# Performance work log

Measured on AMD Instinct MI355X. Metric: run time of the kernel, lower is better.

The kernel has to match this reference:

```python
import jax, jax.numpy as jnp
from jax import lax
import numpy as np

B, ENC, H, DE, T = 16384, 512, 256, 32, 64


def setup_inputs() -> dict:
    key = jax.random.key(0)
    ks = jax.random.split(key, 12)
    s = lambda fan: 1.0 / np.sqrt(fan)
    return {
        "encoded_input_series": jax.random.normal(ks[0], (B, ENC), jnp.float32),
        "final_x_val": jax.random.normal(ks[1], (B, 1), jnp.float32),
        # embed_func: Dense(DE) applied to scalar input (last dim = 1)
        "W_emb": jax.random.normal(ks[2], (1, DE), jnp.float32) * s(1),
        "b_emb": jnp.zeros((DE,), jnp.float32),
        # encode_reshape layer: Dense(H) on encoded series -> initial h
        "W_enc": jax.random.normal(ks[3], (ENC, H), jnp.float32) * s(ENC),
        "b_enc": jnp.zeros((H,), jnp.float32),
        # LSTM cell params (Keras gate order i, f, c, o)
        "W_k": jax.random.normal(ks[4], (DE, 4 * H), jnp.float32) * s(DE),
        "W_r": jax.random.normal(ks[5], (H, 4 * H), jnp.float32) * s(H),
        "b_lstm": jnp.concatenate([jnp.zeros((H,)), jnp.ones((H,)), jnp.zeros((2 * H,))]).astype(jnp.float32),
        # reduce layer: Dense(1)
        "W_red": jax.random.normal(ks[6], (H, 1), jnp.float32) * s(H),
        "b_red": jnp.zeros((1,), jnp.float32),
        "decode_length": T,
    }


def reference(encoded_input_series, final_x_val, W_emb, b_emb, W_enc, b_enc,
              W_k, W_r, b_lstm, W_red, b_red, decode_length):
    Hdim = W_r.shape[0]
    # initial hidden state from encoder summary; cell state zero-initialized
    h0 = encoded_input_series @ W_enc + b_enc            # [B, H]
    c0 = jnp.zeros_like(h0)
    # initial decoder input: embed of last observed value
    x0 = final_x_val @ W_emb + b_emb                     # [B, DE]

    def step(carry, _):
        h, c, x = carry
        gates = x @ W_k + h @ W_r + b_lstm               # [B, 4H]
        i, f, cb, o = jnp.split(gates, 4, axis=-1)
        c_new = jax.nn.sigmoid(f) * c + jax.nn.sigmoid(i) * jnp.tanh(cb)
        h_new = jax.nn.sigmoid(o) * jnp.tanh(c_new)
        y = h_new @ W_red + b_red                        # [B, 1]
        x_next = y @ W_emb + b_emb
        return (h_new, c_new, x_next), y[:, 0]

    _, ys = lax.scan(step, (h0, c0, x0), None, length=decode_length)
    return ys.T                                          # [B, T]
```

## Files before the change

### kernel.cpp

```cpp
#include <hip/hip_runtime.h>
#include <hip/hip_bf16.h>
#include <math.h>


typedef _Float16 f16x8 __attribute__((ext_vector_type(8)));
typedef float f32x4 __attribute__((ext_vector_type(4)));

#define DEV __device__ __forceinline__

constexpr int ENC = 512;
constexpr int HD  = 256;
constexpr int DE  = 32;
constexpr int TT  = 64;
constexpr int NG  = 4 * HD;
constexpr int NKT = 8;
constexpr int TS  = 528;
constexpr int BR  = 32;
constexpr int NMT = 2;
constexpr int BPS = 12;
constexpr int WRS = 36;

constexpr float L2E = 1.44269504088896f;

DEV bool is_f32(const void* blstm) {
  return ((const unsigned*)blstm)[256] == 0x3F800000u;
}
DEV float ldf(const void* p, size_t i, bool f32) {
  return f32 ? ((const float*)p)[i]
             : __bfloat162float(((const __hip_bfloat16*)p)[i]);
}
DEV float gscale(int n) {
  return ((n >> 8) == 2) ? (2.0f * L2E) : L2E;
}
DEV void split2h(float v, _Float16& hi, _Float16& lo) {
  hi = (_Float16)v;
  lo = (_Float16)(v - (float)hi);
}
DEV void ld8cvt2h(const void* p, size_t i, bool f32, f16x8& hi, f16x8& lo) {
  if (f32) {
    const f32x4* q = (const f32x4*)((const float*)p + i);
    f32x4 u0 = q[0], u1 = q[1];
#pragma unroll
    for (int j = 0; j < 4; ++j) {
      float a = u0[j], b = u1[j];
      _Float16 ah = (_Float16)a, bh = (_Float16)b;
      hi[j] = ah; hi[4 + j] = bh;
      lo[j] = (_Float16)(a - (float)ah); lo[4 + j] = (_Float16)(b - (float)bh);
    }
  } else {
    const __hip_bfloat16* s = (const __hip_bfloat16*)p + i;
#pragma unroll
    for (int j = 0; j < 8; ++j) {
      float a = __bfloat162float(s[j]);
      _Float16 ah = (_Float16)a;
      hi[j] = ah;
      lo[j] = (_Float16)(a - (float)ah);
    }
  }
}
DEV f16x8 load8h(const _Float16* p) {
  return *reinterpret_cast<const f16x8*>(p);
}

DEV void waitflag(volatile int* f, int v) {
  while (*f < v) { __builtin_amdgcn_s_sleep(1); }
  asm volatile("" ::: "memory");
}
DEV void signalflag(volatile int* f, int v, int lane) {
  asm volatile("s_waitcnt lgkmcnt(0)" ::: "memory");
  if (lane == 0) *f = v;
}

__global__ __launch_bounds__(256) void pack_vec(const void* __restrict__ wemb,
                                                const void* __restrict__ bemb,
                                                const void* __restrict__ wk,
                                                const void* __restrict__ bl,
                                                const void* __restrict__ bredp,
                                                float* __restrict__ wk2n,
                                                float* __restrict__ wk2s,
                                                float* __restrict__ bps,
                                                float* __restrict__ bp2P) {
  const bool f32 = is_f32(bl);
  int n = blockIdx.x * 256 + threadIdx.x;
  if (n >= NG) return;
  float s1 = 0.f, s2 = 0.f;
  for (int j = 0; j < DE; ++j) {
    float wkv = ldf(wk, (size_t)j * NG + n, f32);
    s1 += ldf(wemb, j, f32) * wkv;
    s2 += ldf(bemb, j, f32) * wkv;
  }
  float b = s2 + ldf(bl, n, f32);
  float sc = gscale(n);
  wk2n[n] = s1;
  wk2s[n] = s1 * sc;
  bps[n]  = b * sc;
  int g = n >> 8, rem = n & 255;
  int hh = (rem >> 4) & 1;
  int cbase = (rem & 0xE0) | (rem & 15);
  int nf = g * 2 + hh;
  bp2P[cbase * BPS + nf] = (b + ldf(bredp, 0, f32) * s1) * sc;
}

__global__ __launch_bounds__(256) void pack_w(const void* __restrict__ wr,
                                              const void* __restrict__ bl,
                                              const void* __restrict__ wred,
                                              const float* __restrict__ wk2n,
                                              _Float16* __restrict__ d0,
                                              _Float16* __restrict__ d1) {
  const bool f32 = is_f32(bl);
  int idx = blockIdx.x * 256 + threadIdx.x;
  if (idx >= NKT * 64 * 64) return;
  int lane = idx & 63, tile = idx >> 6;
  int nt = tile & 63, ks = tile >> 6;
  int kb = ks * 32 + ((lane >> 4) << 3);
  int n  = (nt << 4) + (lane & 15);
  float wn = wk2n[n];
  float sc = gscale(n);
#pragma unroll
  for (int j = 0; j < 8; ++j) {
    int k = kb + j;
    float v = ldf(wr, (size_t)k * NG + n, f32);
    d0[idx * 8 + j] = (_Float16)(v * sc);
    d1[idx * 8 + j] = (_Float16)((v + ldf(wred, k, f32) * wn) * sc);
  }
}

__global__ __launch_bounds__(256) void pack_e(const void* __restrict__ we,
                                              const void* __restrict__ bl,
                                              _Float16* __restrict__ dhi,
                                              _Float16* __restrict__ dlo) {
  const bool f32 = is_f32(bl);
  int idx = blockIdx.x * 256 + threadIdx.x;
  if (idx >= 16 * 16 * 64) return;
  int lane = idx & 63, tile = idx >> 6;
  int nt = tile & 15, ks = tile >> 4;
  int kb = ks * 32 + ((lane >> 4) << 3);
  int n  = (nt << 4) + (lane & 15);
#pragma unroll
  for (int j = 0; j < 8; ++j) {
    float v = ldf(we, (size_t)(kb + j) * HD + n, f32);
    _Float16 h, l;
    split2h(v, h, l);
    dhi[idx * 8 + j] = h;
    dlo[idx * 8 + j] = l;
  }
}

__global__ __launch_bounds__(512)
__attribute__((amdgpu_waves_per_eu(4, 4)))
void lstm_main(
    const void* __restrict__ enc,
    const void* __restrict__ fx,
    const void* __restrict__ benc,
    const void* __restrict__ blstm,
    const void* __restrict__ wred,
    const void* __restrict__ bredp,
    const _Float16* __restrict__ pW0,
    const _Float16* __restrict__ pW1,
    const _Float16* __restrict__ pEhi,
    const _Float16* __restrict__ pElo,
    const float* __restrict__ wk2s,
    const float* __restrict__ bps,
    const float* __restrict__ bp2P,
    const int* __restrict__ dlen,
    void* __restrict__ out) {
  __shared__ __align__(16) _Float16 frag[2][NMT * NKT * TS];
  __shared__ __align__(16) float bp0L[NG];
  __shared__ __align__(16) float wk2L[NG];
  __shared__ __align__(16) float bp2P_l[HD * BPS];
  __shared__ __align__(16) float wredfP[16 * WRS];
  __shared__ __align__(16) float fxL[BR];
  __shared__ int flagv[NKT];

  const bool f32 = is_f32(blstm);
  const int tid  = threadIdx.x;
  const int w    = tid >> 6;
  const int lane = tid & 63;
  const int q    = lane >> 4;
  const int cl   = lane & 15;
  const int r0   = blockIdx.x * BR;
  int Tn = dlen[0];
  if (Tn < 1 || Tn > TT) Tn = TT;

  const int aoff = lane * 8;
  const int hwb = w * TS + q * 32 + 128 * (cl >> 3) + (cl & 7);
  const int cbase = w * 32 + cl;

  const int yrow  = tid >> 4, ypart = tid & 15;
  const int ybase = ((yrow >> 4) * NKT + (ypart >> 1)) * TS +
                    ((yrow & 15) + 16 * ((ypart & 1) * 2)) * 8;
  const int yws   = ypart * WRS;

  if (tid < HD) wredfP[(tid >> 4) * WRS + (tid & 15)] = ldf(wred, tid, f32);
  if (tid < BR) fxL[tid] = ldf(fx, r0 + tid, f32);
  if (tid < NKT) flagv[tid] = 0;
  bp0L[tid]        = bps[tid];
  bp0L[tid + 512]  = bps[tid + 512];
  wk2L[tid]        = wk2s[tid];
  wk2L[tid + 512]  = wk2s[tid + 512];
#pragma unroll
  for (int k = 0; k < HD * BPS / 512; ++k)
    bp2P_l[tid + k * 512] = bp2P[tid + k * 512];
  const float bredf = ldf(bredp, 0, f32);

  f32x4 acc0[NMT][2];
  {
    float be0 = ldf(benc, w * 32 + cl, f32);
    float be1 = ldf(benc, w * 32 + 16 + cl, f32);
#pragma unroll
    for (int mt = 0; mt < NMT; ++mt) {
      acc0[mt][0] = (f32x4){be0, be0, be0, be0};
      acc0[mt][1] = (f32x4){be1, be1, be1, be1};
    }
  }
  const size_t ebase = ((size_t)(w * 2) * 64 + lane) * 8;
#pragma unroll 1
  for (int ks = 0; ks < ENC / 32; ++ks) {
    f16x8 bh[2], bl2[2];
#pragma unroll
    for (int hh = 0; hh < 2; ++hh) {
      size_t fo = ebase + (size_t)(ks * 16 + hh) * 512;
      bh[hh]  = load8h(pEhi + fo);
      bl2[hh] = load8h(pElo + fo);
    }
#pragma unroll
    for (int mt = 0; mt < NMT; ++mt) {
      f16x8 ah, al;
      ld8cvt2h(enc, (size_t)(r0 + mt * 16 + cl) * ENC + ks * 32 + q * 8, f32, ah, al);
#pragma unroll
      for (int hh = 0; hh < 2; ++hh) {
        acc0[mt][hh] = __builtin_amdgcn_mfma_f32_16x16x32_f16(ah, bh[hh],  acc0[mt][hh], 0, 0, 0);
        acc0[mt][hh] = __builtin_amdgcn_mfma_f32_16x16x32_f16(al, bh[hh],  acc0[mt][hh], 0, 0, 0);
        acc0[mt][hh] = __builtin_amdgcn_mfma_f32_16x16x32_f16(ah, bl2[hh], acc0[mt][hh], 0, 0, 0);
      }
    }
  }
#pragma unroll
  for (int mt = 0; mt < NMT; ++mt)
#pragma unroll
    for (int hh = 0; hh < 2; ++hh)
#pragma unroll
      for (int r = 0; r < 4; ++r) {
        int idx = mt * NKT * TS + hwb + r * 8 + hh * 256;
        frag[0][idx] = (_Float16)acc0[mt][hh][r];
      }

  f32x4 cst[NMT][2];
#pragma unroll
  for (int mt = 0; mt < NMT; ++mt)
#pragma unroll
    for (int hh = 0; hh < 2; ++hh) cst[mt][hh] = (f32x4){0.f, 0.f, 0.f, 0.f};

  __syncthreads();

  const _Float16* wbase0 = pW0 + ((size_t)(w * 2) * 64 + lane) * 8;
  const _Float16* wbase1 = pW1 + ((size_t)(w * 2) * 64 + lane) * 8;

#pragma unroll 1
  for (int t = 0; t < Tn; ++t) {
    const _Float16* FH = &frag[t & 1][0];
    _Float16* WH = &frag[(t + 1) & 1][0];

    f32x4 acc[NMT][8];
    if (t == 0) {
      f32x4 fxv[NMT];
#pragma unroll
      for (int mt = 0; mt < NMT; ++mt)
        fxv[mt] = *(const f32x4*)&fxL[mt * 16 + q * 4];
#pragma unroll
      for (int nf = 0; nf < 8; ++nf) {
        int col = (nf >> 1) * 256 + (nf & 1) * 16 + cbase;
        float bb = bp0L[col], wv = wk2L[col];
#pragma unroll
        for (int mt = 0; mt < NMT; ++mt) {
          f32x4 a;
#pragma unroll
          for (int r = 0; r < 4; ++r) a[r] = bb + fxv[mt][r] * wv;
          acc[mt][nf] = a;
        }
      }
    } else {
      f32x4 bA = *(const f32x4*)&bp2P_l[cbase * BPS];
      f32x4 bB = *(const f32x4*)&bp2P_l[cbase * BPS + 4];
#pragma unroll
      for (int nf = 0; nf < 8; ++nf) {
        float bb = (nf < 4) ? bA[nf & 3] : bB[nf & 3];
#pragma unroll
        for (int mt = 0; mt < NMT; ++mt) acc[mt][nf] = (f32x4){bb, bb, bb, bb};
      }
    }

    const _Float16* wb = (t == 0) ? wbase0 : wbase1;
#pragma unroll 1
    for (int j = 0; j < 8; ++j) {
      int ks = (j + w) & 7;
      if (j > 0) waitflag(&flagv[ks], t);
#pragma unroll
      for (int half = 0; half < 2; ++half) {
        f16x8 bc[4];
#pragma unroll
        for (int p = 0; p < 4; ++p)
          bc[p] = load8h(wb +
                         (size_t)(ks * 64 + (half * 2 + (p >> 1)) * 16 + (p & 1)) * 512);
#pragma unroll
        for (int mt = 0; mt < NMT; ++mt) {
          f16x8 ah = load8h(&FH[(mt * NKT + ks) * TS + aoff]);
          __builtin_amdgcn_s_setprio(1);
#pragma unroll
          for (int p = 0; p < 4; ++p)
            acc[mt][half * 4 + p] =
                __builtin_amdgcn_mfma_f32_16x16x32_f16(ah, bc[p], acc[mt][half * 4 + p], 0, 0, 0);
          __builtin_amdgcn_s_setprio(0);
        }
      }
    }

    if (t > 0) {
      float sum = 0.f;
#pragma unroll
      for (int jj = 0; jj < 2; ++jj) {
        f16x8 hv = load8h(&FH[ybase + jj * 128]);
        f32x4 wv0 = *(const f32x4*)&wredfP[yws + jj * 8];
        f32x4 wv1 = *(const f32x4*)&wredfP[yws + jj * 8 + 4];
#pragma unroll
        for (int j = 0; j < 4; ++j) {
          sum += (float)hv[j] * wv0[j];
          sum += (float)hv[4 + j] * wv1[j];
        }
      }
      sum += __shfl_xor(sum, 1);
      sum += __shfl_xor(sum, 2);
      sum += __shfl_xor(sum, 4);
      sum += __shfl_xor(sum, 8);
      if (ypart == 0) {
        float y = sum + bredf;
        size_t oi = (size_t)(r0 + yrow) * TT + (t - 1);
        if (f32) ((float*)out)[oi] = y;
        else     ((__hip_bfloat16*)out)[oi] = __float2bfloat16(y);
      }
    }

#pragma unroll
    for (int mt = 0; mt < NMT; ++mt)
#pragma unroll
      for (int hh = 0; hh < 2; ++hh)
#pragma unroll
        for (int r = 0; r < 4; ++r) {
          float gi = acc[mt][0 + hh][r];
          float gf = acc[mt][2 + hh][r];
          float gc = acc[mt][4 + hh][r];
          float go = acc[mt][6 + hh][r];
          float P = __builtin_amdgcn_exp2f(-gi);
          float F = __builtin_amdgcn_exp2f(-gf);
          float Q = __builtin_amdgcn_exp2f(-gc);
          float S = __builtin_amdgcn_exp2f(-go);
          float p1 = 1.0f + P, q1 = 1.0f + Q, f1 = 1.0f + F, s1 = 1.0f + S;
          float pq = p1 * q1;
          float num = cst[mt][hh][r] * pq + (1.0f - Q) * f1;
          float cn  = num * __builtin_amdgcn_rcpf(f1 * pq);
          cst[mt][hh][r] = cn;
          float R = __builtin_amdgcn_exp2f(-2.0f * L2E * cn);
          float hn = (1.0f - R) * __builtin_amdgcn_rcpf(s1 * (1.0f + R));
          int idx = mt * NKT * TS + hwb + r * 8 + hh * 256;
          WH[idx] = (_Float16)hn;
        }
    signalflag(&flagv[w], t + 1, lane);
  }

#pragma unroll 1
  for (int s = 0; s < NKT; ++s) waitflag(&flagv[s], Tn);
  {
    const _Float16* FH = &frag[Tn & 1][0];
    float sum = 0.f;
#pragma unroll
    for (int jj = 0; jj < 2; ++jj) {
      f16x8 hv = load8h(&FH[ybase + jj * 128]);
      f32x4 wv0 = *(const f32x4*)&wredfP[yws + jj * 8];
      f32x4 wv1 = *(const f32x4*)&wredfP[yws + jj * 8 + 4];
#pragma unroll
      for (int j = 0; j < 4; ++j) {
        sum += (float)hv[j] * wv0[j];
        sum += (float)hv[4 + j] * wv1[j];
      }
    }
    sum += __shfl_xor(sum, 1);
    sum += __shfl_xor(sum, 2);
    sum += __shfl_xor(sum, 4);
    sum += __shfl_xor(sum, 8);
    if (ypart == 0) {
      float y = sum + bredf;
      size_t oi = (size_t)(r0 + yrow) * TT + (Tn - 1);
      if (f32) ((float*)out)[oi] = y;
      else     ((__hip_bfloat16*)out)[oi] = __float2bfloat16(y);
    }
  }
}

extern "C" void kernel_launch(void* const* d_in, const int* in_sizes, int n_in,
                              void* d_out, int out_size, void* d_ws, size_t ws_size,
                              hipStream_t stream) {
  const void* enc  = d_in[0];
  const void* fx   = d_in[1];
  const void* wemb = d_in[2];
  const void* bemb = d_in[3];
  const void* wenc = d_in[4];
  const void* benc = d_in[5];
  const void* wk   = d_in[6];
  const void* wr   = d_in[7];
  const void* bl   = d_in[8];
  const void* wred = d_in[9];
  const void* bred = d_in[10];
  const int* dlen  = (const int*)d_in[11];

  _Float16* pW0 = (_Float16*)d_ws;
  _Float16* pW1 = pW0 + NKT * 64 * 64 * 8;
  _Float16* pEhi = pW1 + NKT * 64 * 64 * 8;
  _Float16* pElo = pEhi + 16 * 16 * 64 * 8;
  float* wk2n = (float*)(pElo + 16 * 16 * 64 * 8);
  float* wk2s = wk2n + NG;
  float* bps  = wk2s + NG;
  float* bp2P = bps + NG;

  pack_vec<<<4, 256, 0, stream>>>(wemb, bemb, wk, bl, bred, wk2n, wk2s, bps, bp2P);
  pack_w<<<128, 256, 0, stream>>>(wr, bl, wred, wk2n, pW0, pW1);
  pack_e<<<64, 256, 0, stream>>>(wenc, bl, pEhi, pElo);

  int nblocks = in_sizes[1] / BR;
  lstm_main<<<nblocks, 512, 0, stream>>>(enc, fx, benc, bl, wred, bred,
                                         pW0, pW1, pEhi, pElo, wk2s, bps, bp2P,
                                         dlen, d_out);
}
```

Baseline: 871.3 us.

## Double rows per block and split hidden columns across sixteen waves

Each block now handles 64 batch rows with 1024 threads, and each of 16 waves owns 16 hidden columns across all four gates, where before 8 waves each owned 32 columns. Each W_r fragment loaded from global memory now feeds four row tiles instead of two, halving weight traffic per row, and the per-column bias/input-weight vectors are repacked gate-interleaved for single vector loads. In exchange there are more waves to synchronise through LDS flags (each k-slice waits on two flags), a larger LDS footprint, and likely lower occupancy per CU.

```diff
diff --git a/kernel.cpp b/kernel.cpp
--- a/kernel.cpp
+++ b/kernel.cpp
@@ -15,9 +15,9 @@
 constexpr int NG  = 4 * HD;
 constexpr int NKT = 8;
 constexpr int TS  = 528;
-constexpr int BR  = 32;
-constexpr int NMT = 2;
-constexpr int BPS = 12;
+constexpr int BR  = 64;
+constexpr int NMT = 4;
+constexpr int NW  = 16;
 constexpr int WRS = 36;
 
 constexpr float L2E = 1.44269504088896f;
@@ -77,8 +77,8 @@
                                                 const void* __restrict__ bl,
                                                 const void* __restrict__ bredp,
                                                 float* __restrict__ wk2n,
-                                                float* __restrict__ wk2s,
-                                                float* __restrict__ bps,
+                                                float* __restrict__ wk2P,
+                                                float* __restrict__ bp0P,
                                                 float* __restrict__ bp2P) {
   const bool f32 = is_f32(bl);
   int n = blockIdx.x * 256 + threadIdx.x;
@@ -91,14 +91,11 @@
   }
   float b = s2 + ldf(bl, n, f32);
   float sc = gscale(n);
+  int g = n >> 8, hcol = n & 255;
   wk2n[n] = s1;
-  wk2s[n] = s1 * sc;
-  bps[n]  = b * sc;
-  int g = n >> 8, rem = n & 255;
-  int hh = (rem >> 4) & 1;
-  int cbase = (rem & 0xE0) | (rem & 15);
-  int nf = g * 2 + hh;
-  bp2P[cbase * BPS + nf] = (b + ldf(bredp, 0, f32) * s1) * sc;
+  wk2P[hcol * 4 + g] = s1 * sc;
+  bp0P[hcol * 4 + g] = b * sc;
+  bp2P[hcol * 4 + g] = (b + ldf(bredp, 0, f32) * s1) * sc;
 }
 
 __global__ __launch_bounds__(256) void pack_w(const void* __restrict__ wr,
@@ -146,7 +143,7 @@
   }
 }
 
-__global__ __launch_bounds__(512)
+__global__ __launch_bounds__(1024)
 __attribute__((amdgpu_waves_per_eu(4, 4)))
 void lstm_main(
     const void* __restrict__ enc,
@@ -159,18 +156,18 @@
     const _Float16* __restrict__ pW1,
     const _Float16* __restrict__ pEhi,
     const _Float16* __restrict__ pElo,
-    const float* __restrict__ wk2s,
-    const float* __restrict__ bps,
+    const float* __restrict__ wk2P,
+    const float* __restrict__ bp0P,
     const float* __restrict__ bp2P,
     const int* __restrict__ dlen,
     void* __restrict__ out) {
   __shared__ __align__(16) _Float16 frag[2][NMT * NKT * TS];
   __shared__ __align__(16) float bp0L[NG];
   __shared__ __align__(16) float wk2L[NG];
-  __shared__ __align__(16) float bp2P_l[HD * BPS];
+  __shared__ __align__(16) float bp2L[NG];
   __shared__ __align__(16) float wredfP[16 * WRS];
   __shared__ __align__(16) float fxL[BR];
-  __shared__ int flagv[NKT];
+  __shared__ int flagv[NW];
 
   const bool f32 = is_f32(blstm);
   const int tid  = threadIdx.x;
@@ -183,8 +180,9 @@
   if (Tn < 1 || Tn > TT) Tn = TT;
 
   const int aoff = lane * 8;
-  const int hwb = w * TS + q * 32 + 128 * (cl >> 3) + (cl & 7);
-  const int cbase = w * 32 + cl;
+  const int hcol = w * 16 + cl;
+  const int hwb = (w >> 1) * TS + q * 32 +
+                  128 * ((w & 1) * 2 + (cl >> 3)) + (cl & 7);
 
   const int yrow  = tid >> 4, ypart = tid & 15;
   const int ybase = ((yrow >> 4) * NKT + (ypart >> 1)) * TS +
@@ -193,125 +191,93 @@
 
   if (tid < HD) wredfP[(tid >> 4) * WRS + (tid & 15)] = ldf(wred, tid, f32);
   if (tid < BR) fxL[tid] = ldf(fx, r0 + tid, f32);
-  if (tid < NKT) flagv[tid] = 0;
-  bp0L[tid]        = bps[tid];
-  bp0L[tid + 512]  = bps[tid + 512];
-  wk2L[tid]        = wk2s[tid];
-  wk2L[tid + 512]  = wk2s[tid + 512];
-#pragma unroll
-  for (int k = 0; k < HD * BPS / 512; ++k)
-    bp2P_l[tid + k * 512] = bp2P[tid + k * 512];
+  if (tid < NW) flagv[tid] = 0;
+  bp0L[tid] = bp0P[tid];
+  bp2L[tid] = bp2P[tid];
+  wk2L[tid] = wk2P[tid];
   const float bredf = ldf(bredp, 0, f32);
 
-  f32x4 acc0[NMT][2];
+  f32x4 acc0[NMT];
   {
-    float be0 = ldf(benc, w * 32 + cl, f32);
-    float be1 = ldf(benc, w * 32 + 16 + cl, f32);
-#pragma unroll
-    for (int mt = 0; mt < NMT; ++mt) {
-      acc0[mt][0] = (f32x4){be0, be0, be0, be0};
-      acc0[mt][1] = (f32x4){be1, be1, be1, be1};
-    }
-  }
-  const size_t ebase = ((size_t)(w * 2) * 64 + lane) * 8;
+    float be = ldf(benc, hcol, f32);
+#pragma unroll
+    for (int mt = 0; mt < NMT; ++mt) acc0[mt] = (f32x4){be, be, be, be};
+  }
+  const size_t ebase = ((size_t)w * 64 + lane) * 8;
 #pragma unroll 1
   for (int ks = 0; ks < ENC / 32; ++ks) {
-    f16x8 bh[2], bl2[2];
-#pragma unroll
-    for (int hh = 0; hh < 2; ++hh) {
-      size_t fo = ebase + (size_t)(ks * 16 + hh) * 512;
-      bh[hh]  = load8h(pEhi + fo);
-      bl2[hh] = load8h(pElo + fo);
-    }
+    size_t fo = ebase + (size_t)(ks * 16) * 512;
+    f16x8 bh  = load8h(pEhi + fo);
+    f16x8 bl2 = load8h(pElo + fo);
 #pragma unroll
     for (int mt = 0; mt < NMT; ++mt) {
       f16x8 ah, al;
       ld8cvt2h(enc, (size_t)(r0 + mt * 16 + cl) * ENC + ks * 32 + q * 8, f32, ah, al);
-#pragma unroll
-      for (int hh = 0; hh < 2; ++hh) {
-        acc0[mt][hh] = __builtin_amdgcn_mfma_f32_16x16x32_f16(ah, bh[hh],  acc0[mt][hh], 0, 0, 0);
-        acc0[mt][hh] = __builtin_amdgcn_mfma_f32_16x16x32_f16(al, bh[hh],  acc0[mt][hh], 0, 0, 0);
-        acc0[mt][hh] = __builtin_amdgcn_mfma_f32_16x16x32_f16(ah, bl2[hh], acc0[mt][hh], 0, 0, 0);
-      }
+      acc0[mt] = __builtin_amdgcn_mfma_f32_16x16x32_f16(ah, bh,  acc0[mt], 0, 0, 0);
+      acc0[mt] = __builtin_amdgcn_mfma_f32_16x16x32_f16(al, bh,  acc0[mt], 0, 0, 0);
+      acc0[mt] = __builtin_amdgcn_mfma_f32_16x16x32_f16(ah, bl2, acc0[mt], 0, 0, 0);
     }
   }
 #pragma unroll
   for (int mt = 0; mt < NMT; ++mt)
 #pragma unroll
-    for (int hh = 0; hh < 2; ++hh)
-#pragma unroll
-      for (int r = 0; r < 4; ++r) {
-        int idx = mt * NKT * TS + hwb + r * 8 + hh * 256;
-        frag[0][idx] = (_Float16)acc0[mt][hh][r];
-      }
-
-  f32x4 cst[NMT][2];
-#pragma unroll
-  for (int mt = 0; mt < NMT; ++mt)
-#pragma unroll
-    for (int hh = 0; hh < 2; ++hh) cst[mt][hh] = (f32x4){0.f, 0.f, 0.f, 0.f};
+    for (int r = 0; r < 4; ++r)
+      frag[0][mt * NKT * TS + hwb + r * 8] = (_Float16)acc0[mt][r];
+
+  f32x4 cst[NMT];
+#pragma unroll
+  for (int mt = 0; mt < NMT; ++mt) cst[mt] = (f32x4){0.f, 0.f, 0.f, 0.f};
 
   __syncthreads();
 
-  const _Float16* wbase0 = pW0 + ((size_t)(w * 2) * 64 + lane) * 8;
-  const _Float16* wbase1 = pW1 + ((size_t)(w * 2) * 64 + lane) * 8;
+  const _Float16* wbase0 = pW0 + ((size_t)w * 64 + lane) * 8;
+  const _Float16* wbase1 = pW1 + ((size_t)w * 64 + lane) * 8;
 
 #pragma unroll 1
   for (int t = 0; t < Tn; ++t) {
     const _Float16* FH = &frag[t & 1][0];
     _Float16* WH = &frag[(t + 1) & 1][0];
 
-    f32x4 acc[NMT][8];
+    f32x4 acc[NMT][4];
     if (t == 0) {
-      f32x4 fxv[NMT];
+      f32x4 b0 = *(const f32x4*)&bp0L[hcol * 4];
+      f32x4 wk = *(const f32x4*)&wk2L[hcol * 4];
 #pragma unroll
       for (int mt = 0; mt < NMT; ++mt)
-        fxv[mt] = *(const f32x4*)&fxL[mt * 16 + q * 4];
-#pragma unroll
-      for (int nf = 0; nf < 8; ++nf) {
-        int col = (nf >> 1) * 256 + (nf & 1) * 16 + cbase;
-        float bb = bp0L[col], wv = wk2L[col];
-#pragma unroll
-        for (int mt = 0; mt < NMT; ++mt) {
-          f32x4 a;
-#pragma unroll
-          for (int r = 0; r < 4; ++r) a[r] = bb + fxv[mt][r] * wv;
-          acc[mt][nf] = a;
+#pragma unroll
+        for (int r = 0; r < 4; ++r) {
+          float fxr = fxL[mt * 16 + q * 4 + r];
+#pragma unroll
+          for (int g = 0; g < 4; ++g) acc[mt][g][r] = b0[g] + fxr * wk[g];
         }
-      }
     } else {
-      f32x4 bA = *(const f32x4*)&bp2P_l[cbase * BPS];
-      f32x4 bB = *(const f32x4*)&bp2P_l[cbase * BPS + 4];
-#pragma unroll
-      for (int nf = 0; nf < 8; ++nf) {
-        float bb = (nf < 4) ? bA[nf & 3] : bB[nf & 3];
-#pragma unroll
-        for (int mt = 0; mt < NMT; ++mt) acc[mt][nf] = (f32x4){bb, bb, bb, bb};
-      }
+      f32x4 bb = *(const f32x4*)&bp2L[hcol * 4];
+#pragma unroll
+      for (int g = 0; g < 4; ++g)
+#pragma unroll
+        for (int mt = 0; mt < NMT; ++mt)
+          acc[mt][g] = (f32x4){bb[g], bb[g], bb[g], bb[g]};
     }
 
     const _Float16* wb = (t == 0) ? wbase0 : wbase1;
 #pragma unroll 1
     for (int j = 0; j < 8; ++j) {
-      int ks = (j + w) & 7;
-      if (j > 0) waitflag(&flagv[ks], t);
-#pragma unroll
-      for (int half = 0; half < 2; ++half) {
-        f16x8 bc[4];
-#pragma unroll
-        for (int p = 0; p < 4; ++p)
-          bc[p] = load8h(wb +
-                         (size_t)(ks * 64 + (half * 2 + (p >> 1)) * 16 + (p & 1)) * 512);
-#pragma unroll
-        for (int mt = 0; mt < NMT; ++mt) {
-          f16x8 ah = load8h(&FH[(mt * NKT + ks) * TS + aoff]);
-          __builtin_amdgcn_s_setprio(1);
-#pragma unroll
-          for (int p = 0; p < 4; ++p)
-            acc[mt][half * 4 + p] =
-                __builtin_amdgcn_mfma_f32_16x16x32_f16(ah, bc[p], acc[mt][half * 4 + p], 0, 0, 0);
-          __builtin_amdgcn_s_setprio(0);
-        }
+      int ks = (j + (w >> 1)) & 7;
+      waitflag(&flagv[2 * ks], t);
+      waitflag(&flagv[2 * ks + 1], t);
+      f16x8 bc[4];
+#pragma unroll
+      for (int g = 0; g < 4; ++g)
+        bc[g] = load8h(wb + (size_t)(ks * 64 + g * 16) * 512);
+#pragma unroll
+      for (int mt = 0; mt < NMT; ++mt) {
+        f16x8 ah = load8h(&FH[(mt * NKT + ks) * TS + aoff]);
+        __builtin_amdgcn_s_setprio(1);
+#pragma unroll
+        for (int g = 0; g < 4; ++g)
+          acc[mt][g] =
+              __builtin_amdgcn_mfma_f32_16x16x32_f16(ah, bc[g], acc[mt][g], 0, 0, 0);
+        __builtin_amdgcn_s_setprio(0);
       }
     }
 
@@ -343,32 +309,29 @@
 #pragma unroll
     for (int mt = 0; mt < NMT; ++mt)
 #pragma unroll
-      for (int hh = 0; hh < 2; ++hh)
-#pragma unroll
-        for (int r = 0; r < 4; ++r) {
-          float gi = acc[mt][0 + hh][r];
-          float gf = acc[mt][2 + hh][r];
-          float gc = acc[mt][4 + hh][r];
-          float go = acc[mt][6 + hh][r];
-          float P = __builtin_amdgcn_exp2f(-gi);
-          float F = __builtin_amdgcn_exp2f(-gf);
-          float Q = __builtin_amdgcn_exp2f(-gc);
-          float S = __builtin_amdgcn_exp2f(-go);
-          float p1 = 1.0f + P, q1 = 1.0f + Q, f1 = 1.0f + F, s1 = 1.0f + S;
-          float pq = p1 * q1;
-          float num = cst[mt][hh][r] * pq + (1.0f - Q) * f1;
-          float cn  = num * __builtin_amdgcn_rcpf(f1 * pq);
-          cst[mt][hh][r] = cn;
-          float R = __builtin_amdgcn_exp2f(-2.0f * L2E * cn);
-          float hn = (1.0f - R) * __builtin_amdgcn_rcpf(s1 * (1.0f + R));
-          int idx = mt * NKT * TS + hwb + r * 8 + hh * 256;
-          WH[idx] = (_Float16)hn;
-        }
+      for (int r = 0; r < 4; ++r) {
+        float gi = acc[mt][0][r];
+        float gf = acc[mt][1][r];
+        float gc = acc[mt][2][r];
+        float go = acc[mt][3][r];
+        float P = __builtin_amdgcn_exp2f(-gi);
+        float F = __builtin_amdgcn_exp2f(-gf);
+        float Q = __builtin_amdgcn_exp2f(-gc);
+        float S = __builtin_amdgcn_exp2f(-go);
+        float p1 = 1.0f + P, q1 = 1.0f + Q, f1 = 1.0f + F, s1 = 1.0f + S;
+        float pq = p1 * q1;
+        float num = cst[mt][r] * pq + (1.0f - Q) * f1;
+        float cn  = num * __builtin_amdgcn_rcpf(f1 * pq);
+        cst[mt][r] = cn;
+        float R = __builtin_amdgcn_exp2f(-2.0f * L2E * cn);
+        float hn = (1.0f - R) * __builtin_amdgcn_rcpf(s1 * (1.0f + R));
+        WH[mt * NKT * TS + hwb + r * 8] = (_Float16)hn;
+      }
     signalflag(&flagv[w], t + 1, lane);
   }
 
 #pragma unroll 1
-  for (int s = 0; s < NKT; ++s) waitflag(&flagv[s], Tn);
+  for (int s = 0; s < NW; ++s) waitflag(&flagv[s], Tn);
   {
     const _Float16* FH = &frag[Tn & 1][0];
     float sum = 0.f;
@@ -417,16 +380,16 @@
   _Float16* pEhi = pW1 + NKT * 64 * 64 * 8;
   _Float16* pElo = pEhi + 16 * 16 * 64 * 8;
   float* wk2n = (float*)(pElo + 16 * 16 * 64 * 8);
-  float* wk2s = wk2n + NG;
-  float* bps  = wk2s + NG;
-  float* bp2P = bps + NG;
-
-  pack_vec<<<4, 256, 0, stream>>>(wemb, bemb, wk, bl, bred, wk2n, wk2s, bps, bp2P);
+  float* wk2P = wk2n + NG;
+  float* bp0P = wk2P + NG;
+  float* bp2P = bp0P + NG;
+
+  pack_vec<<<4, 256, 0, stream>>>(wemb, bemb, wk, bl, bred, wk2n, wk2P, bp0P, bp2P);
   pack_w<<<128, 256, 0, stream>>>(wr, bl, wred, wk2n, pW0, pW1);
   pack_e<<<64, 256, 0, stream>>>(wenc, bl, pEhi, pElo);
 
   int nblocks = in_sizes[1] / BR;
-  lstm_main<<<nblocks, 512, 0, stream>>>(enc, fx, benc, bl, wred, bred,
-                                         pW0, pW1, pEhi, pElo, wk2s, bps, bp2P,
-                                         dlen, d_out);
-}
+  lstm_main<<<nblocks, 1024, 0, stream>>>(enc, fx, benc, bl, wred, bred,
+                                          pW0, pW1, pEhi, pElo, wk2P, bp0P,
+                                          bp2P, dlen, d_out);
+}
```

Result: faster. 779.9 us (-10.5%).
